# Kernel optimization log

Hardware: AMD Instinct MI355X
Metric: run time of the kernel (lower is better)

Reference implementation:

```python
import jax, jax.numpy as jnp
import numpy as np

D_MODEL = 2048
HIDDEN = int(2 * D_MODEL * 4 / 3)  # 5461


def ternary_quant(w):
    # BitNet b1.58-style per-tensor ternary quantization with STE.
    s = jnp.mean(jnp.abs(w))
    q = jnp.clip(jnp.round(w / s), -1.0, 1.0) * s
    return w + jax.lax.stop_gradient(q - w)


def setup_inputs() -> dict:
    key = jax.random.key(0)
    k0, k1, k2, k3 = jax.random.split(key, 4)
    x = jax.random.normal(k0, (4, 4096, D_MODEL), dtype=jnp.float32)
    # torch nn.Linear weights are [out_features, in_features]
    std_in = 1.0 / np.sqrt(D_MODEL)
    std_h = 1.0 / np.sqrt(HIDDEN)
    w1 = jax.random.uniform(k1, (HIDDEN, D_MODEL), jnp.float32, -std_in, std_in)
    w3 = jax.random.uniform(k2, (HIDDEN, D_MODEL), jnp.float32, -std_in, std_in)
    w2 = jax.random.uniform(k3, (D_MODEL, HIDDEN), jnp.float32, -std_h, std_h)
    return {"x": x, "w1": w1, "w3": w3, "w2": w2}


def reference(x, w1, w3, w2):
    w1q = ternary_quant(w1)
    w3q = ternary_quant(w3)
    w2q = ternary_quant(w2)
    h1 = jnp.einsum("bsd,hd->bsh", x, w1q)  # [B,S,H]
    h3 = jnp.einsum("bsd,hd->bsh", x, w3q)  # [B,S,H]
    g = jax.nn.silu(h1) * h3
    return jnp.einsum("bsh,dh->bsd", g, w2q)  # [B,S,D]
```

## Files before the change

kernel.cpp:

```cpp
#include <hip/hip_runtime.h>
#include <cmath>

typedef unsigned short u16;
typedef unsigned char u8;
typedef unsigned int u32;
typedef float f32x4 __attribute__((ext_vector_type(4)));
typedef int i32x4 __attribute__((ext_vector_type(4)));
typedef short s16x8 __attribute__((ext_vector_type(8)));
typedef u32 u32x4 __attribute__((ext_vector_type(4)));

#define D_MODEL 2048
#define HIDDEN  5461
#define HPAD    5504
#define WCNT    11184128
#define XSCALE  4096.0f

__device__ __forceinline__ u16 f2bf(float f) {
  union { float f; u32 u; } c; c.f = f;
  u32 u = c.u + 0x7fffu + ((c.u >> 16) & 1u);
  return (u16)(u >> 16);
}

__device__ __forceinline__ void async16(const void* g, void* l) {
  __builtin_amdgcn_global_load_lds(
      (const __attribute__((address_space(1))) unsigned int*)g,
      (__attribute__((address_space(3))) unsigned int*)l, 16, 0, 0);
}

__global__ void zero_sums_kernel(double* __restrict__ s) {
  if (threadIdx.x < 3) s[threadIdx.x] = 0.0;
}

__global__ void abssum_kernel(const float* __restrict__ w, long n, double* __restrict__ out) {
  long i0 = ((long)blockIdx.x * blockDim.x + threadIdx.x) * 4;
  long stride = (long)gridDim.x * blockDim.x * 4;
  double s = 0.0;
  for (long i = i0; i < n; i += stride) {
    float4 v = *(const float4*)(w + i);
    s += (double)fabsf(v.x) + (double)fabsf(v.y) + (double)fabsf(v.z) + (double)fabsf(v.w);
  }
#pragma unroll
  for (int off = 32; off > 0; off >>= 1) s += __shfl_down(s, off, 64);
  __shared__ double ls[4];
  int lane = threadIdx.x & 63, wv = threadIdx.x >> 6;
  if (lane == 0) ls[wv] = s;
  __syncthreads();
  if (threadIdx.x == 0) atomicAdd(out, ls[0] + ls[1] + ls[2] + ls[3]);
}

__global__ void quant13_kernel(const float* __restrict__ w, const double* __restrict__ sum,
                               char* __restrict__ ws) {
  double s = *sum * (1.0 / (double)WCNT);
  int nt = blockIdx.x;
  int c  = blockIdx.y * 256 + threadIdx.x;
  int col = c & 63;
  int kg  = c >> 6;
  int n = nt * 64 + col;
  u32x4 qv = {0u, 0u, 0u, 0u};
  if (n < HIDDEN) {
    const float* row = w + (long)n * D_MODEL + kg * 16;
#pragma unroll
    for (int q4 = 0; q4 < 4; ++q4) {
      float4 v = *(const float4*)(row + q4 * 4);
      float vv[4] = {v.x, v.y, v.z, v.w};
      u32 word = 0;
#pragma unroll
      for (int e = 0; e < 4; ++e) {
        int qi = (int)fmin(fmax(rint((double)vv[e] / s), -1.0), 1.0);
        word |= ((u32)(u8)(char)qi) << (8 * e);
      }
      qv[q4] = word;
    }
  }
  *(u32x4*)(ws + (long)nt * 131072 + ((long)kg * 64 + col) * 16) = qv;
}

__global__ void quant2_kernel(const float* __restrict__ w, const double* __restrict__ sum,
                              u16* __restrict__ ws) {
  double s = *sum * (1.0 / (double)WCNT);
  int nt = blockIdx.x;
  int kc = blockIdx.y;
  int nn = threadIdx.x & 127;
  int kl = threadIdx.x >> 7;
  int n = nt * 128 + nn;
  long base = (long)nt * 704512;
#pragma unroll
  for (int it = 0; it < 4; ++it) {
    int kgl = kl + it * 2;
    int kg = kc * 8 + kgl;
    s16x8 qv;
#pragma unroll
    for (int j = 0; j < 8; ++j) {
      int k = kg * 8 + j;
      float q = 0.f;
      if (k < HIDDEN) {
        float v = w[(long)n * HIDDEN + k];
        q = (float)fmin(fmax(rint((double)v / s), -1.0), 1.0);
      }
      qv[j] = (short)f2bf(q);
    }
    *(s16x8*)(ws + base + ((long)kg * 128 + nn) * 8) = qv;
  }
}

__global__ void xquant_kernel(const float* __restrict__ x, u8* __restrict__ xhi,
                              u8* __restrict__ xlo) {
  int mt = blockIdx.x;
  int c  = blockIdx.y * 256 + threadIdx.x;
  int row = c & 127;
  int kg  = c >> 7;
  const float* src = x + ((long)mt * 128 + row) * D_MODEL + kg * 16;
  u32x4 hv, lv;
#pragma unroll
  for (int q4 = 0; q4 < 4; ++q4) {
    float4 v = *(const float4*)(src + q4 * 4);
    float vv[4] = {v.x, v.y, v.z, v.w};
    u32 hw = 0, lw = 0;
#pragma unroll
    for (int e = 0; e < 4; ++e) {
      float f = fminf(fmaxf(vv[e] * XSCALE, -32639.f), 32639.f);
      int tt = (int)rintf(f) + 128;
      hw |= ((u32)((tt >> 8) & 0xFF)) << (8 * e);
      lw |= ((u32)((tt ^ 0x80) & 0xFF)) << (8 * e);
    }
    hv[q4] = hw; lv[q4] = lw;
  }
  long o = (long)mt * 262144 + ((long)kg * 128 + row) * 16;
  *(u32x4*)(xhi + o) = hv;
  *(u32x4*)(xlo + o) = lv;
}

__global__ __launch_bounds__(256, 2)
void gemm1_kernel(const u8* __restrict__ xhi, const u8* __restrict__ xlo,
                  const char* __restrict__ w1s, const char* __restrict__ w3s,
                  const double* __restrict__ sums, u16* __restrict__ gs, int mt0) {
  __shared__ alignas(16) u8 L[3 * 24576];
  const int mtl = blockIdx.x;
  const int nt  = blockIdx.y;
  const int mtg = mt0 + mtl;
  const int t = threadIdx.x;
  const int lane = t & 63, wave = t >> 6;
  const int wm = wave >> 1, wn = wave & 1;
  const int quad = lane >> 4;
  const int rowA = wm * 64 + (lane & 15);
  const int rowB = wn * 32 + (lane & 15);

  i32x4 a1h[4][2], a1l[4][2], a3h[4][2], a3l[4][2];
#pragma unroll
  for (int i = 0; i < 4; ++i)
#pragma unroll
    for (int j = 0; j < 2; ++j) {
      a1h[i][j] = {0, 0, 0, 0}; a1l[i][j] = {0, 0, 0, 0};
      a3h[i][j] = {0, 0, 0, 0}; a3l[i][j] = {0, 0, 0, 0};
    }

  const u8* Ah = xhi + (long)mtg * 262144 + t * 16;
  const u8* Al = xlo + (long)mtg * 262144 + t * 16;
  const char* B1 = w1s + (long)nt * 131072 + t * 16;
  const char* B3 = w3s + (long)nt * 131072 + t * 16;

#define STAGE1(buf, c) do {                                      \
    u8* Lb_ = L + (buf) * 24576;                                 \
    async16(Ah + (c) * 8192,        Lb_ + t * 16);               \
    async16(Ah + (c) * 8192 + 4096, Lb_ + 4096 + t * 16);        \
    async16(Al + (c) * 8192,        Lb_ + 8192 + t * 16);        \
    async16(Al + (c) * 8192 + 4096, Lb_ + 12288 + t * 16);       \
    async16(B1 + (c) * 4096,        Lb_ + 16384 + t * 16);       \
    async16(B3 + (c) * 4096,        Lb_ + 20480 + t * 16);       \
  } while (0)

  STAGE1(0, 0);
  int cur = 0;
  for (int c = 0; c < 32; ++c) {
    int nb = cur + 1; if (nb == 3) nb = 0;
    if (c < 31) {
      STAGE1(nb, c + 1);
      asm volatile("s_waitcnt vmcnt(6)" ::: "memory");
    } else {
      asm volatile("s_waitcnt vmcnt(0)" ::: "memory");
    }
    __builtin_amdgcn_s_barrier();
    const u8* Lb = L + cur * 24576;
    i32x4 b1f[2], b3f[2], ah[4], al[4];
#pragma unroll
    for (int j = 0; j < 2; ++j) {
      b1f[j] = *(const i32x4*)&Lb[16384 + quad * 1024 + (rowB + j * 16) * 16];
      b3f[j] = *(const i32x4*)&Lb[20480 + quad * 1024 + (rowB + j * 16) * 16];
    }
#pragma unroll
    for (int i = 0; i < 4; ++i) {
      ah[i] = *(const i32x4*)&Lb[quad * 2048 + (rowA + i * 16) * 16];
      al[i] = *(const i32x4*)&Lb[8192 + quad * 2048 + (rowA + i * 16) * 16];
    }
    __builtin_amdgcn_s_setprio(1);
#pragma unroll
    for (int i = 0; i < 4; ++i)
#pragma unroll
      for (int j = 0; j < 2; ++j) {
        a1h[i][j] = __builtin_amdgcn_mfma_i32_16x16x64_i8(ah[i], b1f[j], a1h[i][j], 0, 0, 0);
        a1l[i][j] = __builtin_amdgcn_mfma_i32_16x16x64_i8(al[i], b1f[j], a1l[i][j], 0, 0, 0);
        a3h[i][j] = __builtin_amdgcn_mfma_i32_16x16x64_i8(ah[i], b3f[j], a3h[i][j], 0, 0, 0);
        a3l[i][j] = __builtin_amdgcn_mfma_i32_16x16x64_i8(al[i], b3f[j], a3l[i][j], 0, 0, 0);
      }
    __builtin_amdgcn_s_setprio(0);
    cur = nb;
  }
#undef STAGE1

  const float sc1 = (float)(sums[0] * (1.0 / (double)WCNT)) / XSCALE;
  const float sc3 = (float)(sums[1] * (1.0 / (double)WCNT)) / XSCALE;
  u16* gb = gs + (long)mtl * 704512;
#pragma unroll
  for (int i = 0; i < 4; ++i) {
#pragma unroll
    for (int j = 0; j < 2; ++j) {
      const int h = nt * 64 + wn * 32 + j * 16 + (lane & 15);
      const int kg2 = h >> 3, jj = h & 7;
#pragma unroll
      for (int rr = 0; rr < 4; ++rr) {
        const int mm = wm * 64 + i * 16 + quad * 4 + rr;
        float h1 = (float)(a1h[i][j][rr] * 256 + a1l[i][j][rr]) * sc1;
        float h3 = (float)(a3h[i][j][rr] * 256 + a3l[i][j][rr]) * sc3;
        float g = (h1 / (1.0f + expf(-h1))) * h3;
        gb[((long)kg2 * 128 + mm) * 8 + jj] = f2bf(g);
      }
    }
  }
}

__global__ __launch_bounds__(256, 2)
void gemm2_kernel(const u16* __restrict__ gs, const u16* __restrict__ w2s,
                  const double* __restrict__ sums, float* __restrict__ out) {
  __shared__ alignas(16) u16 L[3 * 8192];
  const int mt = blockIdx.x, nt = blockIdx.y;
  const int t = threadIdx.x;
  const int lane = t & 63, wave = t >> 6;
  const int wm = wave >> 1, wn = wave & 1;
  const int quad = lane >> 4;
  const int rowA = wm * 64 + (lane & 15);
  const int rowB = wn * 64 + (lane & 15);

  f32x4 acc[4][4];
#pragma unroll
  for (int i = 0; i < 4; ++i)
#pragma unroll
    for (int j = 0; j < 4; ++j) acc[i][j] = {0.f, 0.f, 0.f, 0.f};

  const u16* Ab = gs  + (long)mt * 704512 + t * 8;
  const u16* Bb = w2s + (long)nt * 704512 + t * 8;

#define STAGE2(buf, c) do {                                      \
    u16* Lb_ = L + (buf) * 8192;                                 \
    async16(Ab + (c) * 4096,        Lb_ + t * 8);                \
    async16(Ab + (c) * 4096 + 2048, Lb_ + 2048 + t * 8);         \
    async16(Bb + (c) * 4096,        Lb_ + 4096 + t * 8);         \
    async16(Bb + (c) * 4096 + 2048, Lb_ + 6144 + t * 8);         \
  } while (0)

  STAGE2(0, 0);
  int cur = 0;
  for (int c = 0; c < 172; ++c) {
    int nb = cur + 1; if (nb == 3) nb = 0;
    if (c < 171) {
      STAGE2(nb, c + 1);
      asm volatile("s_waitcnt vmcnt(4)" ::: "memory");
    } else {
      asm volatile("s_waitcnt vmcnt(0)" ::: "memory");
    }
    __builtin_amdgcn_s_barrier();
    const u16* Lb = L + cur * 8192;
    s16x8 af[4], bf[4];
#pragma unroll
    for (int i = 0; i < 4; ++i)
      af[i] = *(const s16x8*)&Lb[quad * 1024 + (rowA + i * 16) * 8];
#pragma unroll
    for (int j = 0; j < 4; ++j)
      bf[j] = *(const s16x8*)&Lb[4096 + quad * 1024 + (rowB + j * 16) * 8];
    __builtin_amdgcn_s_setprio(1);
#pragma unroll
    for (int i = 0; i < 4; ++i)
#pragma unroll
      for (int j = 0; j < 4; ++j)
        acc[i][j] = __builtin_amdgcn_mfma_f32_16x16x32_bf16(af[i], bf[j], acc[i][j], 0, 0, 0);
    __builtin_amdgcn_s_setprio(0);
    cur = nb;
  }
#undef STAGE2

  const float s2 = (float)(sums[2] * (1.0 / (double)WCNT));
#pragma unroll
  for (int i = 0; i < 4; ++i) {
    const int r0 = wm * 64 + i * 16 + quad * 4;
#pragma unroll
    for (int j = 0; j < 4; ++j) {
      const int d = nt * 128 + wn * 64 + j * 16 + (lane & 15);
#pragma unroll
      for (int rr = 0; rr < 4; ++rr) {
        const long m = (long)mt * 128 + r0 + rr;
        out[m * D_MODEL + d] = acc[i][j][rr] * s2;
      }
    }
  }
}

extern "C" void kernel_launch(void* const* d_in, const int* in_sizes, int n_in,
                              void* d_out, int out_size, void* d_ws, size_t ws_size,
                              hipStream_t stream) {
  (void)in_sizes; (void)n_in; (void)out_size; (void)ws_size;
  const float* x  = (const float*)d_in[0];
  const float* w1 = (const float*)d_in[1];
  const float* w3 = (const float*)d_in[2];
  const float* w2 = (const float*)d_in[3];
  float* out = (float*)d_out;

  char* ws = (char*)d_ws;
  double* sums = (double*)ws;
  char* w1s = ws + 256;
  char* w3s = w1s + 11272192L;
  u16*  w2s = (u16*)(w3s + 11272192L);
  u8*   xhi = (u8*)(w3s + 11272192L + 22544384L);
  u8*   xlo = xhi + 33554432L;
  u16*  gs  = (u16*)(xlo + 33554432L);

  zero_sums_kernel<<<1, 64, 0, stream>>>(sums);
  abssum_kernel<<<1024, 256, 0, stream>>>(w1, (long)WCNT, sums + 0);
  abssum_kernel<<<1024, 256, 0, stream>>>(w3, (long)WCNT, sums + 1);
  abssum_kernel<<<1024, 256, 0, stream>>>(w2, (long)WCNT, sums + 2);

  quant13_kernel<<<dim3(86, 32), 256, 0, stream>>>(w1, sums + 0, w1s);
  quant13_kernel<<<dim3(86, 32), 256, 0, stream>>>(w3, sums + 1, w3s);
  quant2_kernel<<<dim3(16, 86), 256, 0, stream>>>(w2, sums + 2, w2s);
  xquant_kernel<<<dim3(128, 64), 256, 0, stream>>>(x, xhi, xlo);

  for (int pass = 0; pass < 2; ++pass) {
    gemm1_kernel<<<dim3(64, 86), 256, 0, stream>>>(xhi, xlo, w1s, w3s, sums, gs, pass * 64);
    gemm2_kernel<<<dim3(64, 16), 256, 0, stream>>>(gs, w2s, sums,
                                                   out + (long)pass * 64 * 128 * D_MODEL);
  }
}
```

Measured before the change: 1.345 ms.

## Quantize gated activations to split int8 and run second GEMM on int8 MFMA

The second GEMM switches from bf16 MFMA to int8 MFMA. The gated activation g is fixed-point quantized into hi and lo int8 bytes, and w2 is stored as ternary int8, so two int8 MFMAs replace one bf16 MFMA at double the K per instruction. Both GEMMs also widen their N tiles: 128 for gemm1 and 256 for gemm2. This doubles the accumulator count and lowers launch bounds to one block per CU, trading occupancy for more reuse per tile. The fixed-point scale of 4096 on g risks clamping or precision loss if activations exceed the representable range, and gemm1 now writes single bytes per element scattered across the output.

```diff
diff --git a/kernel.cpp b/kernel.cpp
--- a/kernel.cpp
+++ b/kernel.cpp
@@ -15,12 +15,6 @@
 #define WCNT    11184128
 #define XSCALE  4096.0f
 
-__device__ __forceinline__ u16 f2bf(float f) {
-  union { float f; u32 u; } c; c.f = f;
-  u32 u = c.u + 0x7fffu + ((c.u >> 16) & 1u);
-  return (u16)(u >> 16);
-}
-
 __device__ __forceinline__ void async16(const void* g, void* l) {
   __builtin_amdgcn_global_load_lds(
       (const __attribute__((address_space(1))) unsigned int*)g,
@@ -53,9 +47,9 @@
   double s = *sum * (1.0 / (double)WCNT);
   int nt = blockIdx.x;
   int c  = blockIdx.y * 256 + threadIdx.x;
-  int col = c & 63;
-  int kg  = c >> 6;
-  int n = nt * 64 + col;
+  int col = c & 127;
+  int kg  = c >> 7;
+  int n = nt * 128 + col;
   u32x4 qv = {0u, 0u, 0u, 0u};
   if (n < HIDDEN) {
     const float* row = w + (long)n * D_MODEL + kg * 16;
@@ -72,35 +66,34 @@
       qv[q4] = word;
     }
   }
-  *(u32x4*)(ws + (long)nt * 131072 + ((long)kg * 64 + col) * 16) = qv;
+  *(u32x4*)(ws + (long)nt * 262144 + ((long)kg * 128 + col) * 16) = qv;
 }
 
 __global__ void quant2_kernel(const float* __restrict__ w, const double* __restrict__ sum,
-                              u16* __restrict__ ws) {
+                              char* __restrict__ ws) {
   double s = *sum * (1.0 / (double)WCNT);
   int nt = blockIdx.x;
-  int kc = blockIdx.y;
-  int nn = threadIdx.x & 127;
-  int kl = threadIdx.x >> 7;
-  int n = nt * 128 + nn;
-  long base = (long)nt * 704512;
-#pragma unroll
-  for (int it = 0; it < 4; ++it) {
-    int kgl = kl + it * 2;
-    int kg = kc * 8 + kgl;
-    s16x8 qv;
-#pragma unroll
-    for (int j = 0; j < 8; ++j) {
-      int k = kg * 8 + j;
-      float q = 0.f;
+  int kg = blockIdx.y;
+  int col = threadIdx.x;
+  int n = nt * 256 + col;
+  const float* row = w + (long)n * HIDDEN;
+  u32x4 qv = {0u, 0u, 0u, 0u};
+#pragma unroll
+  for (int q4 = 0; q4 < 4; ++q4) {
+    u32 word = 0;
+#pragma unroll
+    for (int e = 0; e < 4; ++e) {
+      int k = kg * 16 + q4 * 4 + e;
+      int qi = 0;
       if (k < HIDDEN) {
-        float v = w[(long)n * HIDDEN + k];
-        q = (float)fmin(fmax(rint((double)v / s), -1.0), 1.0);
-      }
-      qv[j] = (short)f2bf(q);
-    }
-    *(s16x8*)(ws + base + ((long)kg * 128 + nn) * 8) = qv;
-  }
+        float v = row[k];
+        qi = (int)fmin(fmax(rint((double)v / s), -1.0), 1.0);
+      }
+      word |= ((u32)(u8)(char)qi) << (8 * e);
+    }
+    qv[q4] = word;
+  }
+  *(u32x4*)(ws + (long)nt * 1409024 + ((long)kg * 256 + col) * 16) = qv;
 }
 
 __global__ void xquant_kernel(const float* __restrict__ x, u8* __restrict__ xhi,
@@ -130,43 +123,45 @@
   *(u32x4*)(xlo + o) = lv;
 }
 
-__global__ __launch_bounds__(256, 2)
+__global__ __launch_bounds__(256, 1)
 void gemm1_kernel(const u8* __restrict__ xhi, const u8* __restrict__ xlo,
                   const char* __restrict__ w1s, const char* __restrict__ w3s,
-                  const double* __restrict__ sums, u16* __restrict__ gs, int mt0) {
-  __shared__ alignas(16) u8 L[3 * 24576];
+                  const double* __restrict__ sums, u8* __restrict__ gshi,
+                  u8* __restrict__ gslo, int mt0) {
+  __shared__ alignas(16) u8 L[3 * 32768];
   const int mtl = blockIdx.x;
-  const int nt  = blockIdx.y;
-  const int mtg = mt0 + mtl;
+  const int ntt = blockIdx.y;
   const int t = threadIdx.x;
   const int lane = t & 63, wave = t >> 6;
   const int wm = wave >> 1, wn = wave & 1;
   const int quad = lane >> 4;
   const int rowA = wm * 64 + (lane & 15);
-  const int rowB = wn * 32 + (lane & 15);
-
-  i32x4 a1h[4][2], a1l[4][2], a3h[4][2], a3l[4][2];
+  const int colB = wn * 64 + (lane & 15);
+
+  i32x4 a1h[4][4], a1l[4][4], a3h[4][4], a3l[4][4];
 #pragma unroll
   for (int i = 0; i < 4; ++i)
 #pragma unroll
-    for (int j = 0; j < 2; ++j) {
+    for (int j = 0; j < 4; ++j) {
       a1h[i][j] = {0, 0, 0, 0}; a1l[i][j] = {0, 0, 0, 0};
       a3h[i][j] = {0, 0, 0, 0}; a3l[i][j] = {0, 0, 0, 0};
     }
 
-  const u8* Ah = xhi + (long)mtg * 262144 + t * 16;
-  const u8* Al = xlo + (long)mtg * 262144 + t * 16;
-  const char* B1 = w1s + (long)nt * 131072 + t * 16;
-  const char* B3 = w3s + (long)nt * 131072 + t * 16;
+  const u8* Ah = xhi + (long)(mt0 + mtl) * 262144 + t * 16;
+  const u8* Al = xlo + (long)(mt0 + mtl) * 262144 + t * 16;
+  const char* B1 = w1s + (long)ntt * 262144 + t * 16;
+  const char* B3 = w3s + (long)ntt * 262144 + t * 16;
 
 #define STAGE1(buf, c) do {                                      \
-    u8* Lb_ = L + (buf) * 24576;                                 \
+    u8* Lb_ = L + (buf) * 32768;                                 \
     async16(Ah + (c) * 8192,        Lb_ + t * 16);               \
     async16(Ah + (c) * 8192 + 4096, Lb_ + 4096 + t * 16);        \
     async16(Al + (c) * 8192,        Lb_ + 8192 + t * 16);        \
     async16(Al + (c) * 8192 + 4096, Lb_ + 12288 + t * 16);       \
-    async16(B1 + (c) * 4096,        Lb_ + 16384 + t * 16);       \
-    async16(B3 + (c) * 4096,        Lb_ + 20480 + t * 16);       \
+    async16(B1 + (c) * 8192,        Lb_ + 16384 + t * 16);       \
+    async16(B1 + (c) * 8192 + 4096, Lb_ + 20480 + t * 16);       \
+    async16(B3 + (c) * 8192,        Lb_ + 24576 + t * 16);       \
+    async16(B3 + (c) * 8192 + 4096, Lb_ + 28672 + t * 16);       \
   } while (0)
 
   STAGE1(0, 0);
@@ -175,28 +170,28 @@
     int nb = cur + 1; if (nb == 3) nb = 0;
     if (c < 31) {
       STAGE1(nb, c + 1);
-      asm volatile("s_waitcnt vmcnt(6)" ::: "memory");
+      asm volatile("s_waitcnt vmcnt(8)" ::: "memory");
     } else {
       asm volatile("s_waitcnt vmcnt(0)" ::: "memory");
     }
     __builtin_amdgcn_s_barrier();
-    const u8* Lb = L + cur * 24576;
-    i32x4 b1f[2], b3f[2], ah[4], al[4];
-#pragma unroll
-    for (int j = 0; j < 2; ++j) {
-      b1f[j] = *(const i32x4*)&Lb[16384 + quad * 1024 + (rowB + j * 16) * 16];
-      b3f[j] = *(const i32x4*)&Lb[20480 + quad * 1024 + (rowB + j * 16) * 16];
+    const u8* Lb = L + cur * 32768;
+    i32x4 ah[4], al[4], b1f[4], b3f[4];
+#pragma unroll
+    for (int j = 0; j < 4; ++j) {
+      b1f[j] = *(const i32x4*)&Lb[16384 + (quad * 128 + colB + j * 16) * 16];
+      b3f[j] = *(const i32x4*)&Lb[24576 + (quad * 128 + colB + j * 16) * 16];
     }
 #pragma unroll
     for (int i = 0; i < 4; ++i) {
-      ah[i] = *(const i32x4*)&Lb[quad * 2048 + (rowA + i * 16) * 16];
-      al[i] = *(const i32x4*)&Lb[8192 + quad * 2048 + (rowA + i * 16) * 16];
+      ah[i] = *(const i32x4*)&Lb[(quad * 128 + rowA + i * 16) * 16];
+      al[i] = *(const i32x4*)&Lb[8192 + (quad * 128 + rowA + i * 16) * 16];
     }
     __builtin_amdgcn_s_setprio(1);
 #pragma unroll
     for (int i = 0; i < 4; ++i)
 #pragma unroll
-      for (int j = 0; j < 2; ++j) {
+      for (int j = 0; j < 4; ++j) {
         a1h[i][j] = __builtin_amdgcn_mfma_i32_16x16x64_i8(ah[i], b1f[j], a1h[i][j], 0, 0, 0);
         a1l[i][j] = __builtin_amdgcn_mfma_i32_16x16x64_i8(al[i], b1f[j], a1l[i][j], 0, 0, 0);
         a3h[i][j] = __builtin_amdgcn_mfma_i32_16x16x64_i8(ah[i], b3f[j], a3h[i][j], 0, 0, 0);
@@ -209,95 +204,113 @@
 
   const float sc1 = (float)(sums[0] * (1.0 / (double)WCNT)) / XSCALE;
   const float sc3 = (float)(sums[1] * (1.0 / (double)WCNT)) / XSCALE;
-  u16* gb = gs + (long)mtl * 704512;
+  u8* gh = gshi + (long)mtl * 704512;
+  u8* gl = gslo + (long)mtl * 704512;
 #pragma unroll
   for (int i = 0; i < 4; ++i) {
 #pragma unroll
-    for (int j = 0; j < 2; ++j) {
-      const int h = nt * 64 + wn * 32 + j * 16 + (lane & 15);
-      const int kg2 = h >> 3, jj = h & 7;
+    for (int j = 0; j < 4; ++j) {
+      const int h = ntt * 128 + wn * 64 + j * 16 + (lane & 15);
+      const long cbase = ((long)(h >> 4) * 128) * 16 + (h & 15);
 #pragma unroll
       for (int rr = 0; rr < 4; ++rr) {
         const int mm = wm * 64 + i * 16 + quad * 4 + rr;
         float h1 = (float)(a1h[i][j][rr] * 256 + a1l[i][j][rr]) * sc1;
         float h3 = (float)(a3h[i][j][rr] * 256 + a3l[i][j][rr]) * sc3;
         float g = (h1 / (1.0f + expf(-h1))) * h3;
-        gb[((long)kg2 * 128 + mm) * 8 + jj] = f2bf(g);
-      }
-    }
-  }
-}
-
-__global__ __launch_bounds__(256, 2)
-void gemm2_kernel(const u16* __restrict__ gs, const u16* __restrict__ w2s,
-                  const double* __restrict__ sums, float* __restrict__ out) {
-  __shared__ alignas(16) u16 L[3 * 8192];
-  const int mt = blockIdx.x, nt = blockIdx.y;
+        float f = fminf(fmaxf(g * XSCALE, -32639.f), 32639.f);
+        int tt2 = (int)rintf(f) + 128;
+        long off = cbase + (long)mm * 16;
+        gh[off] = (u8)((tt2 >> 8) & 0xFF);
+        gl[off] = (u8)((tt2 ^ 0x80) & 0xFF);
+      }
+    }
+  }
+}
+
+__global__ __launch_bounds__(256, 1)
+void gemm2_kernel(const u8* __restrict__ gshi, const u8* __restrict__ gslo,
+                  const char* __restrict__ w2s, const double* __restrict__ sums,
+                  float* __restrict__ out) {
+  __shared__ alignas(16) u8 L[3 * 32768];
+  const int mtl = blockIdx.x;
+  const int ntt = blockIdx.y;
   const int t = threadIdx.x;
   const int lane = t & 63, wave = t >> 6;
   const int wm = wave >> 1, wn = wave & 1;
   const int quad = lane >> 4;
   const int rowA = wm * 64 + (lane & 15);
-  const int rowB = wn * 64 + (lane & 15);
-
-  f32x4 acc[4][4];
+  const int colB = wn * 128 + (lane & 15);
+
+  i32x4 ach[4][8], acl[4][8];
 #pragma unroll
   for (int i = 0; i < 4; ++i)
 #pragma unroll
-    for (int j = 0; j < 4; ++j) acc[i][j] = {0.f, 0.f, 0.f, 0.f};
-
-  const u16* Ab = gs  + (long)mt * 704512 + t * 8;
-  const u16* Bb = w2s + (long)nt * 704512 + t * 8;
+    for (int j = 0; j < 8; ++j) {
+      ach[i][j] = {0, 0, 0, 0}; acl[i][j] = {0, 0, 0, 0};
+    }
+
+  const u8* Ahg = gshi + (long)mtl * 704512 + t * 16;
+  const u8* Alg = gslo + (long)mtl * 704512 + t * 16;
+  const char* Bw = w2s + (long)ntt * 1409024 + t * 16;
 
 #define STAGE2(buf, c) do {                                      \
-    u16* Lb_ = L + (buf) * 8192;                                 \
-    async16(Ab + (c) * 4096,        Lb_ + t * 8);                \
-    async16(Ab + (c) * 4096 + 2048, Lb_ + 2048 + t * 8);         \
-    async16(Bb + (c) * 4096,        Lb_ + 4096 + t * 8);         \
-    async16(Bb + (c) * 4096 + 2048, Lb_ + 6144 + t * 8);         \
+    u8* Lb_ = L + (buf) * 32768;                                 \
+    async16(Ahg + (c) * 8192,         Lb_ + t * 16);             \
+    async16(Ahg + (c) * 8192 + 4096,  Lb_ + 4096 + t * 16);      \
+    async16(Alg + (c) * 8192,         Lb_ + 8192 + t * 16);      \
+    async16(Alg + (c) * 8192 + 4096,  Lb_ + 12288 + t * 16);     \
+    async16(Bw + (c) * 16384,         Lb_ + 16384 + t * 16);     \
+    async16(Bw + (c) * 16384 + 4096,  Lb_ + 20480 + t * 16);     \
+    async16(Bw + (c) * 16384 + 8192,  Lb_ + 24576 + t * 16);     \
+    async16(Bw + (c) * 16384 + 12288, Lb_ + 28672 + t * 16);     \
   } while (0)
 
   STAGE2(0, 0);
   int cur = 0;
-  for (int c = 0; c < 172; ++c) {
+  for (int c = 0; c < 86; ++c) {
     int nb = cur + 1; if (nb == 3) nb = 0;
-    if (c < 171) {
+    if (c < 85) {
       STAGE2(nb, c + 1);
-      asm volatile("s_waitcnt vmcnt(4)" ::: "memory");
+      asm volatile("s_waitcnt vmcnt(8)" ::: "memory");
     } else {
       asm volatile("s_waitcnt vmcnt(0)" ::: "memory");
     }
     __builtin_amdgcn_s_barrier();
-    const u16* Lb = L + cur * 8192;
-    s16x8 af[4], bf[4];
+    const u8* Lb = L + cur * 32768;
+    i32x4 ah[4], al[4], bw[8];
+#pragma unroll
+    for (int j = 0; j < 8; ++j)
+      bw[j] = *(const i32x4*)&Lb[16384 + (quad * 256 + colB + j * 16) * 16];
+#pragma unroll
+    for (int i = 0; i < 4; ++i) {
+      ah[i] = *(const i32x4*)&Lb[(quad * 128 + rowA + i * 16) * 16];
+      al[i] = *(const i32x4*)&Lb[8192 + (quad * 128 + rowA + i * 16) * 16];
+    }
+    __builtin_amdgcn_s_setprio(1);
 #pragma unroll
     for (int i = 0; i < 4; ++i)
-      af[i] = *(const s16x8*)&Lb[quad * 1024 + (rowA + i * 16) * 8];
-#pragma unroll
-    for (int j = 0; j < 4; ++j)
-      bf[j] = *(const s16x8*)&Lb[4096 + quad * 1024 + (rowB + j * 16) * 8];
-    __builtin_amdgcn_s_setprio(1);
-#pragma unroll
-    for (int i = 0; i < 4; ++i)
-#pragma unroll
-      for (int j = 0; j < 4; ++j)
-        acc[i][j] = __builtin_amdgcn_mfma_f32_16x16x32_bf16(af[i], bf[j], acc[i][j], 0, 0, 0);
+#pragma unroll
+      for (int j = 0; j < 8; ++j) {
+        ach[i][j] = __builtin_amdgcn_mfma_i32_16x16x64_i8(ah[i], bw[j], ach[i][j], 0, 0, 0);
+        acl[i][j] = __builtin_amdgcn_mfma_i32_16x16x64_i8(al[i], bw[j], acl[i][j], 0, 0, 0);
+      }
     __builtin_amdgcn_s_setprio(0);
     cur = nb;
   }
 #undef STAGE2
 
-  const float s2 = (float)(sums[2] * (1.0 / (double)WCNT));
+  const float s2g = (float)(sums[2] * (1.0 / (double)WCNT)) / XSCALE;
 #pragma unroll
   for (int i = 0; i < 4; ++i) {
-    const int r0 = wm * 64 + i * 16 + quad * 4;
-#pragma unroll
-    for (int j = 0; j < 4; ++j) {
-      const int d = nt * 128 + wn * 64 + j * 16 + (lane & 15);
+#pragma unroll
+    for (int j = 0; j < 8; ++j) {
+      const int d = ntt * 256 + wn * 128 + j * 16 + (lane & 15);
 #pragma unroll
       for (int rr = 0; rr < 4; ++rr) {
-        const long m = (long)mt * 128 + r0 + rr;
-        out[m * D_MODEL + d] = acc[i][j][rr] * s2;
+        const long m = (long)mtl * 128 + wm * 64 + i * 16 + quad * 4 + rr;
+        int v = ach[i][j][rr] * 256 + acl[i][j][rr];
+        out[m * D_MODEL + d] = (float)v * s2g;
       }
     }
   }
@@ -317,24 +330,26 @@
   double* sums = (double*)ws;
   char* w1s = ws + 256;
   char* w3s = w1s + 11272192L;
-  u16*  w2s = (u16*)(w3s + 11272192L);
-  u8*   xhi = (u8*)(w3s + 11272192L + 22544384L);
+  char* w2s = w3s + 11272192L;
+  u8*   xhi = (u8*)(w2s + 11272192L);
   u8*   xlo = xhi + 33554432L;
-  u16*  gs  = (u16*)(xlo + 33554432L);
+  u8*   gshi = xlo + 33554432L;
+  u8*   gslo = gshi + 45088768L;
 
   zero_sums_kernel<<<1, 64, 0, stream>>>(sums);
   abssum_kernel<<<1024, 256, 0, stream>>>(w1, (long)WCNT, sums + 0);
   abssum_kernel<<<1024, 256, 0, stream>>>(w3, (long)WCNT, sums + 1);
   abssum_kernel<<<1024, 256, 0, stream>>>(w2, (long)WCNT, sums + 2);
 
-  quant13_kernel<<<dim3(86, 32), 256, 0, stream>>>(w1, sums + 0, w1s);
-  quant13_kernel<<<dim3(86, 32), 256, 0, stream>>>(w3, sums + 1, w3s);
-  quant2_kernel<<<dim3(16, 86), 256, 0, stream>>>(w2, sums + 2, w2s);
+  quant13_kernel<<<dim3(43, 64), 256, 0, stream>>>(w1, sums + 0, w1s);
+  quant13_kernel<<<dim3(43, 64), 256, 0, stream>>>(w3, sums + 1, w3s);
+  quant2_kernel<<<dim3(8, 344), 256, 0, stream>>>(w2, sums + 2, w2s);
   xquant_kernel<<<dim3(128, 64), 256, 0, stream>>>(x, xhi, xlo);
 
   for (int pass = 0; pass < 2; ++pass) {
-    gemm1_kernel<<<dim3(64, 86), 256, 0, stream>>>(xhi, xlo, w1s, w3s, sums, gs, pass * 64);
-    gemm2_kernel<<<dim3(64, 16), 256, 0, stream>>>(gs, w2s, sums,
-                                                   out + (long)pass * 64 * 128 * D_MODEL);
-  }
-}
+    gemm1_kernel<<<dim3(64, 43), 256, 0, stream>>>(xhi, xlo, w1s, w3s, sums,
+                                                   gshi, gslo, pass * 64);
+    gemm2_kernel<<<dim3(64, 8), 256, 0, stream>>>(gshi, gslo, w2s, sums,
+                                                  out + (long)pass * 64 * 128 * D_MODEL);
+  }
+}
```

Result: slower. 1.521 ms (+13.1%).
